# Optimization experiments

Measured on AMD Instinct MI355X. Metric: run time of the kernel, lower is better.

The kernel has to match this reference:

```python
import jax, jax.numpy as jnp
import numpy as np

EMBED = 768
HEAD_DIM = 64  # 768 // 12
SEQ = 4096
BATCH = 4


def setup_inputs() -> dict:
    key = jax.random.key(0)
    ks = jax.random.split(key, 7)
    s = 1.0 / np.sqrt(EMBED)
    return {
        "hidden_state": jax.random.normal(ks[0], (BATCH, SEQ, EMBED), dtype=jnp.float32),
        "Wq": jax.random.uniform(ks[1], (EMBED, HEAD_DIM), jnp.float32, -s, s),
        "bq": jax.random.uniform(ks[2], (HEAD_DIM,), jnp.float32, -s, s),
        "Wk": jax.random.uniform(ks[3], (EMBED, HEAD_DIM), jnp.float32, -s, s),
        "bk": jax.random.uniform(ks[4], (HEAD_DIM,), jnp.float32, -s, s),
        "Wv": jax.random.uniform(ks[5], (EMBED, HEAD_DIM), jnp.float32, -s, s),
        "bv": jax.random.uniform(ks[6], (HEAD_DIM,), jnp.float32, -s, s),
    }


def reference(hidden_state, Wq, bq, Wk, bk, Wv, bv):
    # single-head causal attention: QK^T / sqrt(d) -> causal mask -> softmax -> V
    q = hidden_state @ Wq + bq  # [B, S, d]
    k = hidden_state @ Wk + bk
    v = hidden_state @ Wv + bv
    scale = 1.0 / jnp.sqrt(jnp.asarray(HEAD_DIM, dtype=q.dtype))
    scores = jnp.einsum("bqd,bkd->bqk", q, k) * scale  # [B, S, S]
    S = scores.shape[-1]
    causal = jnp.tril(jnp.ones((S, S), dtype=bool))  # tril buffer, mask==0 -> -inf
    scores = jnp.where(causal, scores, -jnp.inf)
    weights = jax.nn.softmax(scores, axis=-1)
    return jnp.einsum("bqk,bkd->bqd", weights, v)  # [B, S, d]
```

## Files before the change

### kernel.cpp

```cpp
#include <hip/hip_runtime.h>
#include <stdint.h>

#define EMBED 768
#define HD 64
#define SEQ 4096
#define BATCH 4
#define NROW (BATCH * SEQ)
#define NBAND (NROW / 64)
#define KSPLIT 8

typedef __bf16 bf16x8 __attribute__((ext_vector_type(8)));
typedef __bf16 bf16x4 __attribute__((ext_vector_type(4)));
typedef float f32x4 __attribute__((ext_vector_type(4)));

__global__ __launch_bounds__(256)
void wconv_kernel(const float* __restrict__ Wq, const float* __restrict__ Wk,
                  const float* __restrict__ Wv, __bf16* __restrict__ wT) {
    int id = blockIdx.x * 256 + threadIdx.x;
    int c = id / EMBED, k = id - c * EMBED;
    const float* W = (c < 64) ? Wq : (c < 128) ? Wk : Wv;
    wT[id] = (__bf16)W[(size_t)k * HD + (c & 63)];
}

__global__ __launch_bounds__(64)
void qkv_gemm_kernel(const float* __restrict__ hidden, const __bf16* __restrict__ wT,
                     const float* __restrict__ bq, const float* __restrict__ bk,
                     const float* __restrict__ bv,
                     __bf16* __restrict__ qo, __bf16* __restrict__ ko,
                     __bf16* __restrict__ vto) {
    const int mat = blockIdx.y;
    const int m0  = blockIdx.x * 16;
    const int lane = threadIdx.x, lr = lane & 15, lg = lane >> 4;

    f32x4 acc[4];
    #pragma unroll
    for (int n = 0; n < 4; ++n) acc[n] = (f32x4){0.f, 0.f, 0.f, 0.f};

    const float*  hrow  = hidden + (size_t)(m0 + lr) * EMBED + lg * 8;
    const __bf16* wbase = wT + (size_t)mat * 64 * EMBED + lg * 8;

    for (int k0 = 0; k0 < EMBED; k0 += 64) {
        bf16x8 a[2];
        #pragma unroll
        for (int ks = 0; ks < 2; ++ks) {
            float4 h0 = *(const float4*)(hrow + k0 + ks * 32);
            float4 h1 = *(const float4*)(hrow + k0 + ks * 32 + 4);
            bf16x8 tv;
            tv[0] = (__bf16)h0.x; tv[1] = (__bf16)h0.y; tv[2] = (__bf16)h0.z; tv[3] = (__bf16)h0.w;
            tv[4] = (__bf16)h1.x; tv[5] = (__bf16)h1.y; tv[6] = (__bf16)h1.z; tv[7] = (__bf16)h1.w;
            a[ks] = tv;
        }
        #pragma unroll
        for (int n = 0; n < 4; ++n) {
            #pragma unroll
            for (int ks = 0; ks < 2; ++ks) {
                bf16x8 bb = *(const bf16x8*)(wbase + (size_t)(n * 16 + lr) * EMBED + k0 + ks * 32);
                acc[n] = __builtin_amdgcn_mfma_f32_16x16x32_bf16(a[ks], bb, acc[n], 0, 0, 0);
            }
        }
    }

    const float* bias = (mat == 0) ? bq : (mat == 1) ? bk : bv;
    const int row0 = m0 + lg * 4;
    if (mat < 2) {
        __bf16* out = (mat == 0) ? qo : ko;
        #pragma unroll
        for (int n = 0; n < 4; ++n) {
            const float bb = bias[n * 16 + lr];
            #pragma unroll
            for (int r = 0; r < 4; ++r)
                out[(size_t)(row0 + r) * HD + n * 16 + lr] = (__bf16)(acc[n][r] + bb);
        }
    } else {
        #pragma unroll
        for (int n = 0; n < 4; ++n) {
            const float bb = bias[n * 16 + lr];
            bf16x4 pv;
            pv[0] = (__bf16)(acc[n][0] + bb);
            pv[1] = (__bf16)(acc[n][1] + bb);
            pv[2] = (__bf16)(acc[n][2] + bb);
            pv[3] = (__bf16)(acc[n][3] + bb);
            *(bf16x4*)&vto[(size_t)(n * 16 + lr) * NROW + row0] = pv;
        }
    }
}

__global__ __launch_bounds__(256)
void attn_kernel(const __bf16* __restrict__ qg, const __bf16* __restrict__ kg,
                 const __bf16* __restrict__ vtg,
                 float* __restrict__ opart, float* __restrict__ ml) {
    __shared__ __bf16 p_lds[4][16][72];

    const int bid = blockIdx.x;
    const int gi  = bid >> 3;
    const int sp  = bid & (KSPLIT - 1);
    const int t   = 63 - (gi >> 2);
    const int b   = gi & 3;
    const int q0b = t * 64;
    const int nkb = q0b + 64;
    const int chunk = ((nkb + 511) >> 9) << 6;
    const int kb = sp * chunk;

    const int w    = threadIdx.x >> 6;
    const int lane = threadIdx.x & 63, lr = lane & 15, lg = lane >> 4;
    const int q0 = q0b + w * 16;
    const int nk = q0 + 16;
    const int ke = (kb + chunk < nk) ? (kb + chunk) : nk;

    float* mlp = ml + ((size_t)gi * KSPLIT + sp) * 128;
    const int rb = w * 16 + lg * 4;

    if (kb >= ke) {
        if (lr == 0) {
            #pragma unroll
            for (int r = 0; r < 4; ++r) mlp[64 + rb + r] = 0.f;
        }
        return;
    }

    const __bf16* qb = qg  + (size_t)b * SEQ * HD;
    const __bf16* kp = kg  + (size_t)b * SEQ * HD;
    const __bf16* vb = vtg + (size_t)b * SEQ;

    const bf16x8 qf0 = *(const bf16x8*)&qb[(q0 + lr) * HD + lg * 8];
    const bf16x8 qf1 = *(const bf16x8*)&qb[(q0 + lr) * HD + 32 + lg * 8];

    f32x4 acc[4];
    const f32x4 zero4 = {0.f, 0.f, 0.f, 0.f};
    #pragma unroll
    for (int n = 0; n < 4; ++n) acc[n] = zero4;
    float m[4], lsum[4];
    #pragma unroll
    for (int r = 0; r < 4; ++r) { m[r] = -INFINITY; lsum[r] = 0.f; }

    const float sc = 0.18033688011112042f;

    for (int kb0 = kb; kb0 < ke; kb0 += 64) {
        f32x4 sj[4];
        #pragma unroll
        for (int j = 0; j < 4; ++j) {
            bf16x8 kf0 = *(const bf16x8*)&kp[(size_t)(kb0 + j * 16 + lr) * HD + lg * 8];
            bf16x8 kf1 = *(const bf16x8*)&kp[(size_t)(kb0 + j * 16 + lr) * HD + 32 + lg * 8];
            f32x4 z = zero4;
            z = __builtin_amdgcn_mfma_f32_16x16x32_bf16(qf0, kf0, z, 0, 0, 0);
            z = __builtin_amdgcn_mfma_f32_16x16x32_bf16(qf1, kf1, z, 0, 0, 0);
            sj[j] = z;
        }

        float tt[4][4];
        #pragma unroll
        for (int j = 0; j < 4; ++j)
            #pragma unroll
            for (int r = 0; r < 4; ++r) tt[j][r] = sj[j][r] * sc;

        if (kb0 + 63 > q0) {
            #pragma unroll
            for (int j = 0; j < 4; ++j)
                #pragma unroll
                for (int r = 0; r < 4; ++r)
                    if (kb0 + j * 16 + lr > q0 + lg * 4 + r) tt[j][r] = -1e30f;
        }

        float mx[4];
        #pragma unroll
        for (int r = 0; r < 4; ++r)
            mx[r] = fmaxf(fmaxf(tt[0][r], tt[1][r]), fmaxf(tt[2][r], tt[3][r]));
        #pragma unroll
        for (int off = 1; off < 16; off <<= 1)
            #pragma unroll
            for (int r = 0; r < 4; ++r) mx[r] = fmaxf(mx[r], __shfl_xor(mx[r], off));

        float p[4][4], rs[4], so[4];
        #pragma unroll
        for (int r = 0; r < 4; ++r) {
            const float nm = fmaxf(m[r], mx[r]);
            so[r] = __builtin_exp2f(m[r] - nm);
            m[r] = nm;
            float a = 0.f;
            #pragma unroll
            for (int j = 0; j < 4; ++j) { p[j][r] = __builtin_exp2f(tt[j][r] - nm); a += p[j][r]; }
            rs[r] = a;
        }
        #pragma unroll
        for (int off = 1; off < 16; off <<= 1)
            #pragma unroll
            for (int r = 0; r < 4; ++r) rs[r] += __shfl_xor(rs[r], off);
        #pragma unroll
        for (int r = 0; r < 4; ++r) lsum[r] = lsum[r] * so[r] + rs[r];
        #pragma unroll
        for (int n = 0; n < 4; ++n)
            #pragma unroll
            for (int r = 0; r < 4; ++r) acc[n][r] *= so[r];

        #pragma unroll
        for (int j = 0; j < 4; ++j)
            #pragma unroll
            for (int r = 0; r < 4; ++r)
                p_lds[w][lg * 4 + r][j * 16 + lr] = (__bf16)p[j][r];
        asm volatile("s_waitcnt lgkmcnt(0)" ::: "memory");
        const bf16x8 pa0 = *(const bf16x8*)&p_lds[w][lr][lg * 8];
        const bf16x8 pa1 = *(const bf16x8*)&p_lds[w][lr][32 + lg * 8];
        #pragma unroll
        for (int n = 0; n < 4; ++n) {
            bf16x8 vf0 = *(const bf16x8*)&vb[(size_t)(n * 16 + lr) * NROW + kb0 + lg * 8];
            acc[n] = __builtin_amdgcn_mfma_f32_16x16x32_bf16(pa0, vf0, acc[n], 0, 0, 0);
            bf16x8 vf1 = *(const bf16x8*)&vb[(size_t)(n * 16 + lr) * NROW + kb0 + 32 + lg * 8];
            acc[n] = __builtin_amdgcn_mfma_f32_16x16x32_bf16(pa1, vf1, acc[n], 0, 0, 0);
        }
        asm volatile("" ::: "memory");
    }

    float* Op = opart + (size_t)(gi * KSPLIT + sp) * (64 * 64);
    #pragma unroll
    for (int n = 0; n < 4; ++n)
        #pragma unroll
        for (int r = 0; r < 4; ++r)
            Op[(size_t)(rb + r) * 64 + n * 16 + lr] = acc[n][r];
    if (lr == 0) {
        #pragma unroll
        for (int r = 0; r < 4; ++r) {
            mlp[rb + r]      = m[r];
            mlp[64 + rb + r] = (m[r] > -1e29f) ? lsum[r] : 0.f;
        }
    }
}

__global__ __launch_bounds__(256)
void reduce_kernel(const float* __restrict__ opart, const float* __restrict__ ml,
                   float* __restrict__ out) {
    const int e   = blockIdx.x * 256 + threadIdx.x;
    const int col = e & 63;
    const int row = e >> 6;
    const int b   = row >> 12;
    const int sq  = row & (SEQ - 1);
    const int t   = sq >> 6;
    const int gi  = (63 - t) * 4 + b;
    const int r64 = sq & 63;
    const int nkb = (t + 1) * 64;
    const int chunk = ((nkb + 511) >> 9) << 6;
    const int nsp   = (nkb + chunk - 1) / chunk;

    float M = -INFINITY, ls = 0.f, o = 0.f;
    for (int sp = 0; sp < nsp; ++sp) {
        const size_t base = (size_t)gi * KSPLIT + sp;
        const float lv = ml[base * 128 + 64 + r64];
        if (lv > 0.f) {
            const float mv = ml[base * 128 + r64];
            const float nm = fmaxf(M, mv);
            const float f0 = __builtin_exp2f(M - nm);
            const float f1 = __builtin_exp2f(mv - nm);
            const float ov = opart[base * (64 * 64) + (size_t)r64 * 64 + col];
            o  = o * f0 + f1 * ov;
            ls = ls * f0 + f1 * lv;
            M = nm;
        }
    }
    out[e] = o / ls;
}

extern "C" void kernel_launch(void* const* d_in, const int* in_sizes, int n_in,
                              void* d_out, int out_size, void* d_ws, size_t ws_size,
                              hipStream_t stream) {
    const float* hidden = (const float*)d_in[0];
    const float* Wq = (const float*)d_in[1];
    const float* bq = (const float*)d_in[2];
    const float* Wk = (const float*)d_in[3];
    const float* bk = (const float*)d_in[4];
    const float* Wv = (const float*)d_in[5];
    const float* bv = (const float*)d_in[6];

    __bf16* qbuf  = (__bf16*)d_ws;
    __bf16* kbuf  = qbuf + (size_t)NROW * HD;
    __bf16* vtbuf = kbuf + (size_t)NROW * HD;
    __bf16* wT    = vtbuf + (size_t)NROW * HD;
    float*  opart = (float*)(wT + (size_t)192 * EMBED);
    float*  ml    = opart + (size_t)NBAND * KSPLIT * 64 * 64;

    wconv_kernel<<<(192 * EMBED) / 256, 256, 0, stream>>>(Wq, Wk, Wv, wT);

    qkv_gemm_kernel<<<dim3(NROW / 16, 3), 64, 0, stream>>>(
        hidden, wT, bq, bk, bv, qbuf, kbuf, vtbuf);

    attn_kernel<<<NBAND * KSPLIT, 256, 0, stream>>>(
        qbuf, kbuf, vtbuf, opart, ml);

    reduce_kernel<<<(NROW * HD) / 256, 256, 0, stream>>>(opart, ml, (float*)d_out);
}
```

Baseline: 225.4 us.

## Use fixed 256-key chunks for attention split and merge QKV GEMM into one block

```diff
diff --git a/kernel.cpp b/kernel.cpp
--- a/kernel.cpp
+++ b/kernel.cpp
@@ -6,8 +6,8 @@
 #define SEQ 4096
 #define BATCH 4
 #define NROW (BATCH * SEQ)
-#define NBAND (NROW / 64)
-#define KSPLIT 8
+#define MAXCH 16
+#define NDENSE 2176
 
 typedef __bf16 bf16x8 __attribute__((ext_vector_type(8)));
 typedef __bf16 bf16x4 __attribute__((ext_vector_type(4)));
@@ -22,22 +22,21 @@
     wT[id] = (__bf16)W[(size_t)k * HD + (c & 63)];
 }
 
-__global__ __launch_bounds__(64)
+__global__ __launch_bounds__(256, 4)
 void qkv_gemm_kernel(const float* __restrict__ hidden, const __bf16* __restrict__ wT,
                      const float* __restrict__ bq, const float* __restrict__ bk,
                      const float* __restrict__ bv,
                      __bf16* __restrict__ qo, __bf16* __restrict__ ko,
                      __bf16* __restrict__ vto) {
-    const int mat = blockIdx.y;
-    const int m0  = blockIdx.x * 16;
-    const int lane = threadIdx.x, lr = lane & 15, lg = lane >> 4;
-
-    f32x4 acc[4];
-    #pragma unroll
-    for (int n = 0; n < 4; ++n) acc[n] = (f32x4){0.f, 0.f, 0.f, 0.f};
-
-    const float*  hrow  = hidden + (size_t)(m0 + lr) * EMBED + lg * 8;
-    const __bf16* wbase = wT + (size_t)mat * 64 * EMBED + lg * 8;
+    const int m0 = blockIdx.x * 16;
+    const int w  = threadIdx.x >> 6;
+    const int lane = threadIdx.x & 63, lr = lane & 15, lg = lane >> 4;
+
+    f32x4 acc[3];
+    #pragma unroll
+    for (int j = 0; j < 3; ++j) acc[j] = (f32x4){0.f, 0.f, 0.f, 0.f};
+
+    const float* hrow = hidden + (size_t)(m0 + lr) * EMBED + lg * 8;
 
     for (int k0 = 0; k0 < EMBED; k0 += 64) {
         bf16x8 a[2];
@@ -51,72 +50,74 @@
             a[ks] = tv;
         }
         #pragma unroll
-        for (int n = 0; n < 4; ++n) {
+        for (int j = 0; j < 3; ++j) {
+            const int col = w * 48 + j * 16 + lr;
             #pragma unroll
             for (int ks = 0; ks < 2; ++ks) {
-                bf16x8 bb = *(const bf16x8*)(wbase + (size_t)(n * 16 + lr) * EMBED + k0 + ks * 32);
-                acc[n] = __builtin_amdgcn_mfma_f32_16x16x32_bf16(a[ks], bb, acc[n], 0, 0, 0);
+                bf16x8 bb = *(const bf16x8*)(wT + (size_t)col * EMBED + k0 + ks * 32 + lg * 8);
+                acc[j] = __builtin_amdgcn_mfma_f32_16x16x32_bf16(a[ks], bb, acc[j], 0, 0, 0);
             }
         }
     }
 
-    const float* bias = (mat == 0) ? bq : (mat == 1) ? bk : bv;
+    const float qsc = 0.18033688011112042f;
     const int row0 = m0 + lg * 4;
-    if (mat < 2) {
-        __bf16* out = (mat == 0) ? qo : ko;
-        #pragma unroll
-        for (int n = 0; n < 4; ++n) {
-            const float bb = bias[n * 16 + lr];
+    #pragma unroll
+    for (int j = 0; j < 3; ++j) {
+        const int cw  = w * 48 + j * 16;
+        const int mat = cw >> 6;
+        const int cm  = (cw & 63) + lr;
+        if (mat == 0) {
+            const float bb = bq[cm];
             #pragma unroll
             for (int r = 0; r < 4; ++r)
-                out[(size_t)(row0 + r) * HD + n * 16 + lr] = (__bf16)(acc[n][r] + bb);
-        }
-    } else {
-        #pragma unroll
-        for (int n = 0; n < 4; ++n) {
-            const float bb = bias[n * 16 + lr];
+                qo[(size_t)(row0 + r) * HD + cm] = (__bf16)((acc[j][r] + bb) * qsc);
+        } else if (mat == 1) {
+            const float bb = bk[cm];
+            #pragma unroll
+            for (int r = 0; r < 4; ++r)
+                ko[(size_t)(row0 + r) * HD + cm] = (__bf16)(acc[j][r] + bb);
+        } else {
+            const float bb = bv[cm];
             bf16x4 pv;
-            pv[0] = (__bf16)(acc[n][0] + bb);
-            pv[1] = (__bf16)(acc[n][1] + bb);
-            pv[2] = (__bf16)(acc[n][2] + bb);
-            pv[3] = (__bf16)(acc[n][3] + bb);
-            *(bf16x4*)&vto[(size_t)(n * 16 + lr) * NROW + row0] = pv;
-        }
-    }
-}
-
-__global__ __launch_bounds__(256)
+            pv[0] = (__bf16)(acc[j][0] + bb);
+            pv[1] = (__bf16)(acc[j][1] + bb);
+            pv[2] = (__bf16)(acc[j][2] + bb);
+            pv[3] = (__bf16)(acc[j][3] + bb);
+            *(bf16x4*)&vto[(size_t)cm * NROW + row0] = pv;
+        }
+    }
+}
+
+__device__ __forceinline__ int band_cum(int t) {
+    const int A = t >> 2, r = t & 3;
+    return (A + 1) * (2 * A + r);
+}
+
+__global__ __launch_bounds__(256, 8)
 void attn_kernel(const __bf16* __restrict__ qg, const __bf16* __restrict__ kg,
                  const __bf16* __restrict__ vtg,
                  float* __restrict__ opart, float* __restrict__ ml) {
     __shared__ __bf16 p_lds[4][16][72];
 
-    const int bid = blockIdx.x;
-    const int gi  = bid >> 3;
-    const int sp  = bid & (KSPLIT - 1);
-    const int t   = 63 - (gi >> 2);
-    const int b   = gi & 3;
+    const int y = blockIdx.y;
+    const int t = 63 - (y >> 2);
+    const int b = y & 3;
+    const int c = blockIdx.x;
+    if (c > (t >> 2)) return;
+
     const int q0b = t * 64;
-    const int nkb = q0b + 64;
-    const int chunk = ((nkb + 511) >> 9) << 6;
-    const int kb = sp * chunk;
+    const int kb  = c * 256;
 
     const int w    = threadIdx.x >> 6;
     const int lane = threadIdx.x & 63, lr = lane & 15, lg = lane >> 4;
     const int q0 = q0b + w * 16;
     const int nk = q0 + 16;
-    const int ke = (kb + chunk < nk) ? (kb + chunk) : nk;
-
-    float* mlp = ml + ((size_t)gi * KSPLIT + sp) * 128;
+    const int ke = (kb + 256 < nk) ? (kb + 256) : nk;
+    if (kb >= ke) return;
+
+    const int dense = (band_cum(t) + c) * 4 + b;
     const int rb = w * 16 + lg * 4;
-
-    if (kb >= ke) {
-        if (lr == 0) {
-            #pragma unroll
-            for (int r = 0; r < 4; ++r) mlp[64 + rb + r] = 0.f;
-        }
-        return;
-    }
 
     const __bf16* qb = qg  + (size_t)b * SEQ * HD;
     const __bf16* kp = kg  + (size_t)b * SEQ * HD;
@@ -132,8 +133,6 @@
     float m[4], lsum[4];
     #pragma unroll
     for (int r = 0; r < 4; ++r) { m[r] = -INFINITY; lsum[r] = 0.f; }
-
-    const float sc = 0.18033688011112042f;
 
     for (int kb0 = kb; kb0 < ke; kb0 += 64) {
         f32x4 sj[4];
@@ -147,30 +146,24 @@
             sj[j] = z;
         }
 
-        float tt[4][4];
-        #pragma unroll
-        for (int j = 0; j < 4; ++j)
-            #pragma unroll
-            for (int r = 0; r < 4; ++r) tt[j][r] = sj[j][r] * sc;
-
         if (kb0 + 63 > q0) {
             #pragma unroll
             for (int j = 0; j < 4; ++j)
                 #pragma unroll
                 for (int r = 0; r < 4; ++r)
-                    if (kb0 + j * 16 + lr > q0 + lg * 4 + r) tt[j][r] = -1e30f;
+                    if (kb0 + j * 16 + lr > q0 + lg * 4 + r) sj[j][r] = -1e30f;
         }
 
         float mx[4];
         #pragma unroll
         for (int r = 0; r < 4; ++r)
-            mx[r] = fmaxf(fmaxf(tt[0][r], tt[1][r]), fmaxf(tt[2][r], tt[3][r]));
+            mx[r] = fmaxf(fmaxf(sj[0][r], sj[1][r]), fmaxf(sj[2][r], sj[3][r]));
         #pragma unroll
         for (int off = 1; off < 16; off <<= 1)
             #pragma unroll
             for (int r = 0; r < 4; ++r) mx[r] = fmaxf(mx[r], __shfl_xor(mx[r], off));
 
-        float p[4][4], rs[4], so[4];
+        float rs[4], so[4];
         #pragma unroll
         for (int r = 0; r < 4; ++r) {
             const float nm = fmaxf(m[r], mx[r]);
@@ -178,7 +171,10 @@
             m[r] = nm;
             float a = 0.f;
             #pragma unroll
-            for (int j = 0; j < 4; ++j) { p[j][r] = __builtin_exp2f(tt[j][r] - nm); a += p[j][r]; }
+            for (int j = 0; j < 4; ++j) {
+                sj[j][r] = __builtin_exp2f(sj[j][r] - nm);
+                a += sj[j][r];
+            }
             rs[r] = a;
         }
         #pragma unroll
@@ -196,7 +192,7 @@
         for (int j = 0; j < 4; ++j)
             #pragma unroll
             for (int r = 0; r < 4; ++r)
-                p_lds[w][lg * 4 + r][j * 16 + lr] = (__bf16)p[j][r];
+                p_lds[w][lg * 4 + r][j * 16 + lr] = (__bf16)sj[j][r];
         asm volatile("s_waitcnt lgkmcnt(0)" ::: "memory");
         const bf16x8 pa0 = *(const bf16x8*)&p_lds[w][lr][lg * 8];
         const bf16x8 pa1 = *(const bf16x8*)&p_lds[w][lr][32 + lg * 8];
@@ -210,7 +206,8 @@
         asm volatile("" ::: "memory");
     }
 
-    float* Op = opart + (size_t)(gi * KSPLIT + sp) * (64 * 64);
+    float* Op  = opart + (size_t)dense * (64 * 64);
+    float* mlp = ml + (size_t)dense * 128;
     #pragma unroll
     for (int n = 0; n < 4; ++n)
         #pragma unroll
@@ -234,15 +231,14 @@
     const int b   = row >> 12;
     const int sq  = row & (SEQ - 1);
     const int t   = sq >> 6;
-    const int gi  = (63 - t) * 4 + b;
     const int r64 = sq & 63;
-    const int nkb = (t + 1) * 64;
-    const int chunk = ((nkb + 511) >> 9) << 6;
-    const int nsp   = (nkb + chunk - 1) / chunk;
+    const int nkr = (sq & ~15) + 16;
+    const int nsp = (nkr + 255) >> 8;
+    const int cum = band_cum(t);
 
     float M = -INFINITY, ls = 0.f, o = 0.f;
     for (int sp = 0; sp < nsp; ++sp) {
-        const size_t base = (size_t)gi * KSPLIT + sp;
+        const size_t base = (size_t)(cum + sp) * 4 + b;
         const float lv = ml[base * 128 + 64 + r64];
         if (lv > 0.f) {
             const float mv = ml[base * 128 + r64];
@@ -274,14 +270,14 @@
     __bf16* vtbuf = kbuf + (size_t)NROW * HD;
     __bf16* wT    = vtbuf + (size_t)NROW * HD;
     float*  opart = (float*)(wT + (size_t)192 * EMBED);
-    float*  ml    = opart + (size_t)NBAND * KSPLIT * 64 * 64;
+    float*  ml    = opart + (size_t)NDENSE * 64 * 64;
 
     wconv_kernel<<<(192 * EMBED) / 256, 256, 0, stream>>>(Wq, Wk, Wv, wT);
 
-    qkv_gemm_kernel<<<dim3(NROW / 16, 3), 64, 0, stream>>>(
+    qkv_gemm_kernel<<<NROW / 16, 256, 0, stream>>>(
         hidden, wT, bq, bk, bv, qbuf, kbuf, vtbuf);
 
-    attn_kernel<<<NBAND * KSPLIT, 256, 0, stream>>>(
+    attn_kernel<<<dim3(MAXCH, 256), 256, 0, stream>>>(
         qbuf, kbuf, vtbuf, opart, ml);
 
     reduce_kernel<<<(NROW * HD) / 256, 256, 0, stream>>>(opart, ml, (float*)d_out);
```

Result: slower. 333.8 us (+48.1%).
